# Kernel tuning notes

Hardware: AMD Instinct MI355X
Metric: run time of the kernel (lower is better)

## Reference

```python
import jax, jax.numpy as jnp
import numpy as np

N_NODES = 100000


def gcn_layer(x, row, col, ew, W, b, n_nodes):
    # PyG GCNConv: add self-loops (weight 1), symmetric normalization
    # deg^{-1/2}[row] * w * deg^{-1/2}[col], linear transform, scatter-add to col.
    loop = jnp.arange(n_nodes, dtype=row.dtype)
    row_f = jnp.concatenate([row, loop])
    col_f = jnp.concatenate([col, loop])
    ew_f = jnp.concatenate([ew, jnp.ones((n_nodes,), dtype=ew.dtype)])
    deg = jax.ops.segment_sum(ew_f, col_f, num_segments=n_nodes)  # [N]
    dinv = jnp.where(deg > 0, jax.lax.rsqrt(deg), 0.0)
    norm = dinv[row_f] * ew_f * dinv[col_f]  # [E+N]
    h = x @ W  # [N, F_out]
    msg = norm[:, None] * h[row_f]  # [E+N, F_out]
    out = jax.ops.segment_sum(msg, col_f, num_segments=n_nodes)
    return out + b


def setup_inputs() -> dict:
    key = jax.random.key(0)
    ks = jax.random.split(key, 6)
    n, e, d_in, d_h = N_NODES, 3200000, 128, 16
    x = jax.random.normal(ks[0], (n, d_in), dtype=jnp.float32)
    edge_index = jax.random.randint(ks[1], (2, e), 0, n, dtype=jnp.int64)
    edge_weight = jax.random.uniform(ks[2], (e,), dtype=jnp.float32)
    W1 = jax.random.normal(ks[3], (d_in, d_h), dtype=jnp.float32) * (1.0 / np.sqrt(d_in))
    b1 = jnp.zeros((d_h,), dtype=jnp.float32)
    W2 = jax.random.normal(ks[4], (d_h, 1), dtype=jnp.float32) * (1.0 / np.sqrt(d_h))
    b2 = jnp.zeros((1,), dtype=jnp.float32)
    return {"x": x, "edge_index": edge_index, "edge_weight": edge_weight,
            "W1": W1, "b1": b1, "W2": W2, "b2": b2}


def reference(x, edge_index, edge_weight, W1, b1, W2, b2):
    row, col = edge_index[0], edge_index[1]
    n = x.shape[0]
    h = gcn_layer(x, row, col, edge_weight, W1, b1, n)
    h = jax.nn.relu(h)
    out = gcn_layer(h, row, col, edge_weight, W2, b2, n)
    return out.squeeze(-1)  # [N]
```

## Files before the change

kernel.cpp:

```cpp
#include <hip/hip_runtime.h>
#include <hip/hip_bf16.h>


#define DH 16
#define BSH 6
#define BNODES 64
#define NB_MAX 1568
#define CHUNK 4096
#define HCHUNK 8192
#define NSLICE 4

__global__ __launch_bounds__(256) void k_Ahist(const int* __restrict__ col,
                                               int* __restrict__ gCnt, int E, int NB) {
    __shared__ int lh[NB_MAX];
    const int tid = threadIdx.x;
    for (int i = tid; i < NB; i += 256) lh[i] = 0;
    __syncthreads();
    const int base = blockIdx.x * HCHUNK;
    #pragma unroll
    for (int k = 0; k < 32; ++k) {
        int e = base + tid + 256 * k;
        if (e < E) atomicAdd(&lh[col[e] >> BSH], 1);
    }
    __syncthreads();
    for (int i = tid; i < NB; i += 256) {
        int v = lh[i];
        if (v) atomicAdd(&gCnt[i], v);
    }
}

__global__ __launch_bounds__(1024) void k_Ascan(const int* __restrict__ gCnt,
                                                int* __restrict__ gBase,
                                                int* __restrict__ gCursor,
                                                int NB, int E) {
    __shared__ int s[1024];
    const int t = threadIdx.x;
    const int i0 = 2 * t, i1 = 2 * t + 1;
    int a = (i0 < NB) ? gCnt[i0] : 0;
    int b = (i1 < NB) ? gCnt[i1] : 0;
    int v = a + b;
    s[t] = v;
    __syncthreads();
    for (int off = 1; off < 1024; off <<= 1) {
        int u = (t >= off) ? s[t - off] : 0;
        __syncthreads();
        s[t] += u;
        __syncthreads();
    }
    int ex = s[t] - v;
    if (i0 < NB) { gBase[i0] = ex;     gCursor[i0] = ex; }
    if (i1 < NB) { gBase[i1] = ex + a; gCursor[i1] = ex + a; }
    if (t == 0) gBase[NB] = E;
}

__global__ __launch_bounds__(256) void k_Ascatter(const int* __restrict__ row,
                                                  const int* __restrict__ col,
                                                  const float* __restrict__ ew,
                                                  int* __restrict__ gCursor,
                                                  uint2* __restrict__ edata,
                                                  int E, int NB) {
    __shared__ int lh[NB_MAX];
    __shared__ int lbase[NB_MAX];
    __shared__ int lcur[NB_MAX];
    __shared__ int tsum[256];
    __shared__ unsigned short sbuck[CHUNK];
    __shared__ uint2 stage[CHUNK];
    const int tid = threadIdx.x;
    for (int i = tid; i < NB; i += 256) lh[i] = 0;
    __syncthreads();
    const int base = blockIdx.x * CHUNK;
    int r_[16], c_[16];
    float w_[16];
    #pragma unroll
    for (int k = 0; k < 16; ++k) {
        int e = base + tid + 256 * k;
        bool ok = e < E;
        c_[k] = ok ? col[e] : -1;
        r_[k] = ok ? row[e] : 0;
        w_[k] = ok ? ew[e] : 0.f;
        if (ok) atomicAdd(&lh[c_[k] >> BSH], 1);
    }
    __syncthreads();
    const int t0 = tid * 8;
    int c8[8];
    int mysum = 0;
    #pragma unroll
    for (int k = 0; k < 8; ++k) {
        c8[k] = (t0 + k < NB) ? lh[t0 + k] : 0;
        mysum += c8[k];
    }
    tsum[tid] = mysum;
    __syncthreads();
    for (int off = 1; off < 256; off <<= 1) {
        int u = (tid >= off) ? tsum[tid - off] : 0;
        __syncthreads();
        tsum[tid] += u;
        __syncthreads();
    }
    int p = tsum[tid] - mysum;
    #pragma unroll
    for (int k = 0; k < 8; ++k) {
        if (t0 + k < NB) { lbase[t0 + k] = p; lcur[t0 + k] = p; }
        p += c8[k];
    }
    __syncthreads();
    for (int b = tid; b < NB; b += 256) {
        int cnt = lh[b];
        if (cnt) {
            int g = atomicAdd(&gCursor[b], cnt);
            lh[b] = g - lbase[b];
        }
    }
    __syncthreads();
    #pragma unroll
    for (int k = 0; k < 16; ++k) {
        if (c_[k] >= 0) {
            int b = c_[k] >> BSH;
            unsigned rem = (unsigned)(c_[k] & (BNODES - 1));
            int sp = atomicAdd(&lcur[b], 1);
            stage[sp] = make_uint2((unsigned)r_[k] | (rem << 20), __float_as_uint(w_[k]));
            sbuck[sp] = (unsigned short)b;
        }
    }
    __syncthreads();
    int nE = E - base;
    if (nE > CHUNK) nE = CHUNK;
    for (int j = tid; j < nE; j += 256)
        edata[lh[sbuck[j]] + j] = stage[j];
}

__global__ __launch_bounds__(256) void k_deg(const int* __restrict__ gBase,
                                             const uint2* __restrict__ edata,
                                             float* __restrict__ deg, int N) {
    __shared__ float dg[BNODES];
    const int tid = threadIdx.x;
    if (tid < BNODES) dg[tid] = 0.f;
    __syncthreads();
    const int b = blockIdx.x;
    const int s = gBase[b], e = gBase[b + 1];
    for (int i = s + blockIdx.y * 256 + tid; i < e; i += 512) {
        uint2 ed = edata[i];
        atomicAdd(&dg[ed.x >> 20], __uint_as_float(ed.y));
    }
    __syncthreads();
    int node = (b << BSH) + tid;
    if (tid < BNODES && node < N && dg[tid] != 0.f)
        atomicAdd(&deg[node], dg[tid]);
}

__global__ __launch_bounds__(256) void k_h1(const float* __restrict__ x,
                                            const float* __restrict__ W1,
                                            const float* __restrict__ deg,
                                            float* __restrict__ dinv,
                                            __hip_bfloat16* __restrict__ hdb) {
    __shared__ float Ws[128 * DH];
    __shared__ float xs[16 * 132];
    const int t = threadIdx.x;
    const int node0 = blockIdx.x * 16;
    #pragma unroll
    for (int i = 0; i < 8; ++i) Ws[t + 256 * i] = W1[t + 256 * i];
    const float4* xg = (const float4*)(x + (size_t)node0 * 128);
    #pragma unroll
    for (int it = 0; it < 2; ++it) {
        int idx = t + 256 * it;
        int n = idx >> 5, k4 = idx & 31;
        float4 v = xg[n * 32 + k4];
        *(float4*)(&xs[n * 132 + k4 * 4]) = v;
    }
    __syncthreads();
    const int node = t >> 4, feat = t & 15;
    const float* xr = &xs[node * 132];
    float acc = 0.f;
    #pragma unroll 8
    for (int k = 0; k < 128; ++k) acc += xr[k] * Ws[k * DH + feat];
    const int v = node0 + node;
    const float di = rsqrtf(deg[v] + 1.0f);
    if (feat == 0) dinv[v] = di;
    hdb[(size_t)v * DH + feat] = __float2bfloat16(di * acc);
}

__global__ __launch_bounds__(256) void k_gather1(
    const int* __restrict__ gBase, const uint2* __restrict__ edata,
    const __hip_bfloat16* __restrict__ hdb, float* __restrict__ partial) {
    __shared__ float acc[BNODES][DH + 1];
    const int tid = threadIdx.x;
    for (int i = tid; i < BNODES * (DH + 1); i += 256) ((float*)acc)[i] = 0.f;
    __syncthreads();
    const int b = blockIdx.x, sl = blockIdx.y;
    const int s = gBase[b], e = gBase[b + 1];
    const int g = tid >> 4, f = tid & 15;
    for (int i = s + sl * 16 + g; i < e; i += 256) {
        uint2 e0 = edata[i];
        uint2 e1 = (i + 64  < e) ? edata[i + 64]  : make_uint2(0u, 0u);
        uint2 e2 = (i + 128 < e) ? edata[i + 128] : make_uint2(0u, 0u);
        uint2 e3 = (i + 192 < e) ? edata[i + 192] : make_uint2(0u, 0u);
        float h0 = __bfloat162float(hdb[(size_t)(e0.x & 0xFFFFF) * DH + f]);
        float h1 = __bfloat162float(hdb[(size_t)(e1.x & 0xFFFFF) * DH + f]);
        float h2 = __bfloat162float(hdb[(size_t)(e2.x & 0xFFFFF) * DH + f]);
        float h3 = __bfloat162float(hdb[(size_t)(e3.x & 0xFFFFF) * DH + f]);
        atomicAdd(&acc[e0.x >> 20][f], __uint_as_float(e0.y) * h0);
        atomicAdd(&acc[e1.x >> 20][f], __uint_as_float(e1.y) * h1);
        atomicAdd(&acc[e2.x >> 20][f], __uint_as_float(e2.y) * h2);
        atomicAdd(&acc[e3.x >> 20][f], __uint_as_float(e3.y) * h3);
    }
    __syncthreads();
    float* ps = partial + ((size_t)b * NSLICE + sl) * (DH * BNODES);
    for (int i = tid; i < DH * BNODES; i += 256)
        ps[i] = acc[i >> 4][i & 15];
}

__global__ __launch_bounds__(256) void k_fin1(
    const float* __restrict__ partial, const float* __restrict__ dinv,
    const __hip_bfloat16* __restrict__ hdb, const float* __restrict__ b1,
    const float* __restrict__ W2, const float* __restrict__ b2,
    __hip_bfloat16* __restrict__ qb, float* __restrict__ out, int N) {
    __shared__ float acc[BNODES][DH + 1];
    __shared__ float b1s[DH], W2s[DH];
    const int tid = threadIdx.x;
    if (tid < DH) { b1s[tid] = b1[tid]; W2s[tid] = W2[tid]; }
    const int b = blockIdx.x;
    const float* ps = partial + (size_t)b * NSLICE * (DH * BNODES);
    for (int i = tid; i < DH * BNODES; i += 256) {
        float s = 0.f;
        #pragma unroll
        for (int sl = 0; sl < NSLICE; ++sl) s += ps[sl * (DH * BNODES) + i];
        acc[i >> 4][i & 15] = s;
    }
    __syncthreads();
    int node = (b << BSH) + tid;
    if (tid < BNODES && node < N) {
        float dc = dinv[node];
        const __hip_bfloat16* hs = hdb + (size_t)node * DH;
        float t = 0.f;
        #pragma unroll
        for (int f = 0; f < DH; ++f) {
            float hv = __bfloat162float(hs[f]);
            t += fmaxf(dc * (acc[tid][f] + hv) + b1s[f], 0.f) * W2s[f];
        }
        float qq = dc * t;
        qb[node] = __float2bfloat16(qq);
        out[node] = b2[0] + dc * qq;
    }
}

__global__ __launch_bounds__(256) void k_gather2(
    const int* __restrict__ gBase, const uint2* __restrict__ edata,
    const float* __restrict__ dinv, const __hip_bfloat16* __restrict__ qb,
    float* __restrict__ out, int N) {
    __shared__ float a2[BNODES];
    const int tid = threadIdx.x;
    if (tid < BNODES) a2[tid] = 0.f;
    __syncthreads();
    const int b = blockIdx.x;
    const int s = gBase[b], e = gBase[b + 1];
    for (int i = s + blockIdx.y * 256 + tid; i < e; i += 512) {
        uint2 ed = edata[i];
        float qv = __bfloat162float(qb[ed.x & 0xFFFFF]);
        atomicAdd(&a2[ed.x >> 20], __uint_as_float(ed.y) * qv);
    }
    __syncthreads();
    int node = (b << BSH) + tid;
    if (tid < BNODES && node < N && a2[tid] != 0.f)
        atomicAdd(&out[node], dinv[node] * a2[tid]);
}

extern "C" void kernel_launch(void* const* d_in, const int* in_sizes, int n_in,
                              void* d_out, int out_size, void* d_ws, size_t ws_size,
                              hipStream_t stream) {
    const float* x  = (const float*)d_in[0];
    const int*   ei = (const int*)d_in[1];
    const float* ew = (const float*)d_in[2];
    const float* W1 = (const float*)d_in[3];
    const float* b1 = (const float*)d_in[4];
    const float* W2 = (const float*)d_in[5];
    const float* b2 = (const float*)d_in[6];
    float* out = (float*)d_out;

    const int N = in_sizes[0] / 128;
    const int E = in_sizes[2];
    const int* row = ei;
    const int* col = ei + E;
    const int NB = (N + BNODES - 1) >> BSH;
    const int NBp = (NB + 3) & ~3;

    int* gCnt    = (int*)d_ws;
    float* deg   = (float*)(gCnt + NBp);
    int* gBase   = (int*)(deg + N);
    int* gCursor = gBase + NBp;
    float* dinv  = (float*)(gCursor + NBp);
    __hip_bfloat16* hdb = (__hip_bfloat16*)(dinv + N);
    __hip_bfloat16* qb  = hdb + (size_t)16 * N;
    uintptr_t pp = (uintptr_t)(qb + N);
    pp = (pp + 15) & ~(uintptr_t)15;
    float* partial = (float*)pp;
    uintptr_t ep = (uintptr_t)(partial + (size_t)NB * NSLICE * (DH * BNODES));
    ep = (ep + 15) & ~(uintptr_t)15;
    uint2* edata = (uint2*)ep;

    const int hblocks = (E + HCHUNK - 1) / HCHUNK;
    const int sblocks = (E + CHUNK - 1) / CHUNK;

    hipMemsetAsync(gCnt, 0, ((size_t)NBp + N) * sizeof(int), stream);
    k_Ahist<<<hblocks, 256, 0, stream>>>(col, gCnt, E, NB);
    k_Ascan<<<1, 1024, 0, stream>>>(gCnt, gBase, gCursor, NB, E);
    k_Ascatter<<<sblocks, 256, 0, stream>>>(row, col, ew, gCursor, edata, E, NB);
    k_deg<<<dim3(NB, 2), 256, 0, stream>>>(gBase, edata, deg, N);
    k_h1<<<N / 16, 256, 0, stream>>>(x, W1, deg, dinv, hdb);
    k_gather1<<<dim3(NB, NSLICE), 256, 0, stream>>>(gBase, edata, hdb, partial);
    k_fin1<<<NB, 256, 0, stream>>>(partial, dinv, hdb, b1, W2, b2, qb, out, N);
    k_gather2<<<dim3(NB, 2), 256, 0, stream>>>(gBase, edata, dinv, qb, out, N);
}
```

Measured before the change: 523.6 us.

## Stage edge chunks in LDS and gather packed bf16 pairs in GCN gathers

```diff
diff --git a/kernel.cpp b/kernel.cpp
--- a/kernel.cpp
+++ b/kernel.cpp
@@ -9,6 +9,8 @@
 #define CHUNK 4096
 #define HCHUNK 8192
 #define NSLICE 4
+#define SE_CAP 768
+#define SE2_CAP 1280
 
 __global__ __launch_bounds__(256) void k_Ahist(const int* __restrict__ col,
                                                int* __restrict__ gCnt, int E, int NB) {
@@ -183,25 +185,51 @@
     const int* __restrict__ gBase, const uint2* __restrict__ edata,
     const __hip_bfloat16* __restrict__ hdb, float* __restrict__ partial) {
     __shared__ float acc[BNODES][DH + 1];
+    __shared__ uint2 se[SE_CAP];
     const int tid = threadIdx.x;
     for (int i = tid; i < BNODES * (DH + 1); i += 256) ((float*)acc)[i] = 0.f;
-    __syncthreads();
     const int b = blockIdx.x, sl = blockIdx.y;
     const int s = gBase[b], e = gBase[b + 1];
-    const int g = tid >> 4, f = tid & 15;
-    for (int i = s + sl * 16 + g; i < e; i += 256) {
-        uint2 e0 = edata[i];
-        uint2 e1 = (i + 64  < e) ? edata[i + 64]  : make_uint2(0u, 0u);
-        uint2 e2 = (i + 128 < e) ? edata[i + 128] : make_uint2(0u, 0u);
-        uint2 e3 = (i + 192 < e) ? edata[i + 192] : make_uint2(0u, 0u);
-        float h0 = __bfloat162float(hdb[(size_t)(e0.x & 0xFFFFF) * DH + f]);
-        float h1 = __bfloat162float(hdb[(size_t)(e1.x & 0xFFFFF) * DH + f]);
-        float h2 = __bfloat162float(hdb[(size_t)(e2.x & 0xFFFFF) * DH + f]);
-        float h3 = __bfloat162float(hdb[(size_t)(e3.x & 0xFFFFF) * DH + f]);
-        atomicAdd(&acc[e0.x >> 20][f], __uint_as_float(e0.y) * h0);
-        atomicAdd(&acc[e1.x >> 20][f], __uint_as_float(e1.y) * h1);
-        atomicAdd(&acc[e2.x >> 20][f], __uint_as_float(e2.y) * h2);
-        atomicAdd(&acc[e3.x >> 20][f], __uint_as_float(e3.y) * h3);
+    const int L = e - s;
+    const int per = (L + NSLICE - 1) / NSLICE;
+    const int s0 = s + sl * per;
+    const int e0 = (s0 + per < e) ? (s0 + per) : e;
+    const int g = tid >> 3;
+    const int f2 = tid & 7;
+    const uint* __restrict__ hp = (const uint*)hdb;
+
+    for (int c0 = s0; c0 < e0; c0 += SE_CAP) {
+        const int len = ((e0 - c0) < SE_CAP) ? (e0 - c0) : SE_CAP;
+        __syncthreads();
+        for (int j = tid; j < len; j += 256) se[j] = edata[c0 + j];
+        __syncthreads();
+        const int nfull = len & ~255;
+        for (int j0 = 0; j0 < nfull; j0 += 256) {
+            uint2 ed[8];
+            uint hv[8];
+            #pragma unroll
+            for (int k = 0; k < 8; ++k) ed[k] = se[j0 + g + k * 32];
+            #pragma unroll
+            for (int k = 0; k < 8; ++k)
+                hv[k] = hp[(size_t)(ed[k].x & 0xFFFFFu) * 8 + f2];
+            #pragma unroll
+            for (int k = 0; k < 8; ++k) {
+                const float w = __uint_as_float(ed[k].y);
+                const int rem = ed[k].x >> 20;
+                atomicAdd(&acc[rem][2 * f2],
+                          w * __uint_as_float(hv[k] << 16));
+                atomicAdd(&acc[rem][2 * f2 + 1],
+                          w * __uint_as_float(hv[k] & 0xFFFF0000u));
+            }
+        }
+        for (int j = nfull + g; j < len; j += 32) {
+            const uint2 ed = se[j];
+            const uint hv = hp[(size_t)(ed.x & 0xFFFFFu) * 8 + f2];
+            const float w = __uint_as_float(ed.y);
+            const int rem = ed.x >> 20;
+            atomicAdd(&acc[rem][2 * f2],     w * __uint_as_float(hv << 16));
+            atomicAdd(&acc[rem][2 * f2 + 1], w * __uint_as_float(hv & 0xFFFF0000u));
+        }
     }
     __syncthreads();
     float* ps = partial + ((size_t)b * NSLICE + sl) * (DH * BNODES);
@@ -248,15 +276,41 @@
     const float* __restrict__ dinv, const __hip_bfloat16* __restrict__ qb,
     float* __restrict__ out, int N) {
     __shared__ float a2[BNODES];
+    __shared__ uint2 se[SE2_CAP];
     const int tid = threadIdx.x;
     if (tid < BNODES) a2[tid] = 0.f;
-    __syncthreads();
     const int b = blockIdx.x;
     const int s = gBase[b], e = gBase[b + 1];
-    for (int i = s + blockIdx.y * 256 + tid; i < e; i += 512) {
-        uint2 ed = edata[i];
-        float qv = __bfloat162float(qb[ed.x & 0xFFFFF]);
-        atomicAdd(&a2[ed.x >> 20], __uint_as_float(ed.y) * qv);
+    const int L = e - s;
+    const int per = (L + 1) >> 1;
+    const int s0 = s + blockIdx.y * per;
+    const int e0 = (s0 + per < e) ? (s0 + per) : e;
+    const ushort* __restrict__ qp = (const ushort*)qb;
+
+    for (int c0 = s0; c0 < e0; c0 += SE2_CAP) {
+        const int len = ((e0 - c0) < SE2_CAP) ? (e0 - c0) : SE2_CAP;
+        __syncthreads();
+        for (int j = tid; j < len; j += 256) se[j] = edata[c0 + j];
+        __syncthreads();
+        const int nfull = len & ~1023;
+        for (int j0 = 0; j0 < nfull; j0 += 1024) {
+            uint2 ed[4];
+            uint qv[4];
+            #pragma unroll
+            for (int k = 0; k < 4; ++k) ed[k] = se[j0 + tid + k * 256];
+            #pragma unroll
+            for (int k = 0; k < 4; ++k)
+                qv[k] = (uint)qp[ed[k].x & 0xFFFFFu];
+            #pragma unroll
+            for (int k = 0; k < 4; ++k)
+                atomicAdd(&a2[ed[k].x >> 20],
+                          __uint_as_float(ed[k].y) * __uint_as_float(qv[k] << 16));
+        }
+        for (int j = nfull + tid; j < len; j += 256) {
+            const uint2 ed = se[j];
+            const float q = __uint_as_float((uint)qp[ed.x & 0xFFFFFu] << 16);
+            atomicAdd(&a2[ed.x >> 20], __uint_as_float(ed.y) * q);
+        }
     }
     __syncthreads();
     int node = (b << BSH) + tid;
```

Result: no change. 524.3 us (+0.1%).
